# Performance work log

Hardware: AMD Instinct MI355X
Metric: run time of the kernel (lower is better)

The kernel has to match this reference:

```python
import jax, jax.numpy as jnp
import numpy as np

N_DEPTH = 16  # == serialization_depth init kwarg


def _normalize(v, axis):
    # F.normalize: v / max(||v||, 1e-12)
    return v / jnp.maximum(jnp.linalg.norm(v, axis=axis, keepdims=True), 1e-12)


def _weighted_mean(p, mask):
    # p: [B,N,1], mask: [B,N]
    n = jnp.sum(mask, axis=1, keepdims=True)[..., None]
    return jnp.sum(p * mask[..., None], axis=1, keepdims=True) / (n + 1e-9)


def _select_duplet(points, m, k1, k2):
    # pick 2 random valid points (argmin of rand + big penalty on masked-out) and average
    B, N, _ = points.shape
    def pick(k):
        s = jax.random.uniform(k, (B, N)) + (1.0 - m) * 1e9
        idx = jnp.argmin(s, axis=1)           # [B]
        return jnp.take_along_axis(points, idx[:, None, None], axis=1)  # [B,1,3]
    return (pick(k1) + pick(k2)) * 0.5


def _align(points, ml, mr, ks):
    pl = points - _select_duplet(points, ml, ks[0], ks[1])
    pr = points - _select_duplet(points, mr, ks[2], ks[3])
    return pl * ml[..., None] + pr * mr[..., None]


def _serialize(coords, mask, n_depth, key):
    B, N, _ = coords.shape
    inf = float(2 ** (n_depth // 2 + 3))
    s0 = 2 ** (n_depth // 2 + 1)
    # integer halving each step, exactly like score_scale // 2 in torch
    scales = jnp.asarray(np.array([s0 >> i for i in range(n_depth)], dtype=np.float32))
    keys = jax.random.split(key, n_depth * 5).reshape(n_depth, 5)

    total0 = jnp.zeros((B, N, 1), coords.dtype)
    oldABC0 = jnp.ones((B, 3, 1), coords.dtype)

    def step(carry, inp):
        points, oldABC, total = carry
        ks, scale = inp
        ABC = jax.random.normal(ks[0], (B, 3, 1), coords.dtype)
        angle = jnp.sum(_normalize(ABC, 1) * _normalize(oldABC, 1), axis=1, keepdims=True)
        sgn = jnp.sign(angle)
        sgn = jnp.where(sgn == 0, 1.0, sgn)
        ABC = ABC * sgn
        proj = points @ ABC                    # [B,N,1]
        proj = proj - _weighted_mean(proj, mask)
        score = jnp.sign(proj)                 # [B,N,1]
        total = total + score * scale
        ml = jnp.minimum(jax.nn.relu(-score[..., 0]), mask)
        mr = jnp.minimum(jax.nn.relu(score[..., 0]), mask)
        points = _align(points, ml, mr, ks[1:])
        return (points, ABC, total), None

    (_, _, total), _ = jax.lax.scan(step, (coords, oldABC0, total0), (keys, scales))
    total = total + inf * (1.0 - mask)[..., None]
    return jnp.argsort(total[..., 0], axis=1)  # [B,N]


def setup_inputs() -> dict:
    key = jax.random.key(0)
    k1, k2 = jax.random.split(key)
    B, N, D = 16, 8192, 256
    x = jax.random.normal(k1, (B, N, D), dtype=jnp.float32)
    x_coords = jax.random.normal(k2, (B, N, 3), dtype=jnp.float32)
    mask = jnp.ones((B, N), dtype=jnp.float32)
    return {"x": x, "x_coords": x_coords, "mask": mask}


def reference(x, x_coords, mask):
    key = jax.random.key(42)
    idx = _serialize(x_coords, mask, N_DEPTH, key)   # [B,N] int
    # reverse_indices: gather(arange, idx) == idx, then argsort
    rev = jnp.argsort(idx, axis=1)
    x_out = jnp.take_along_axis(x, idx[:, :, None], axis=1)
    return x_out, rev
```

## Files before the change

kernel.cpp:

```cpp
#include <hip/hip_runtime.h>
#include <stdint.h>

#pragma clang fp contract(off)

constexpr bool kPartitionable = true;

constexpr int B_ = 16;
constexpr int N_ = 8192;
constexpr int TPB = 1024;
constexpr int NSTEP = 10;

__device__ __forceinline__ void tf2x32(uint32_t k0, uint32_t k1,
                                       uint32_t x0, uint32_t x1,
                                       uint32_t& o0, uint32_t& o1) {
  uint32_t ks2 = k0 ^ k1 ^ 0x1BD11BDAu;
  x0 += k0; x1 += k1;
#define RND(r) { x0 += x1; x1 = (x1 << (r)) | (x1 >> (32 - (r))); x1 ^= x0; }
  RND(13) RND(15) RND(26) RND(6)   x0 += k1;  x1 += ks2 + 1u;
  RND(17) RND(29) RND(16) RND(24)  x0 += ks2; x1 += k0  + 2u;
  RND(13) RND(15) RND(26) RND(6)   x0 += k0;  x1 += k1  + 3u;
  RND(17) RND(29) RND(16) RND(24)  x0 += k1;  x1 += ks2 + 4u;
  RND(13) RND(15) RND(26) RND(6)   x0 += ks2; x1 += k0  + 5u;
#undef RND
  o0 = x0; o1 = x1;
}

__device__ __forceinline__ uint32_t rbits(uint32_t k0, uint32_t k1, uint32_t i) {
  uint32_t o0, o1;
  tf2x32(k0, k1, 0u, i, o0, o1);
  return o0 ^ o1;
}

__device__ __forceinline__ void derive_key(uint32_t j, uint32_t& k0, uint32_t& k1) {
  uint32_t o0, o1;
  tf2x32(0u, 42u, 0u, j, o0, o1);
  k0 = o0; k1 = o1;
}

__device__ __forceinline__ float u01_from_bits(uint32_t bits) {
  return __fsub_rn(__uint_as_float((bits >> 9) | 0x3f800000u), 1.0f);
}

__device__ __forceinline__ float xla_logf(float x) {
  uint32_t ix = __float_as_uint(x);
  int e = (int)((ix >> 23) & 0xffu) - 126;
  float m = __uint_as_float((ix & 0x007fffffu) | 0x3f000000u);
  float ef = (float)e;
  if (m < 0.707106781186547524f) {
    ef = __fsub_rn(ef, 1.0f);
    m = __fsub_rn(__fadd_rn(m, m), 1.0f);
  } else {
    m = __fsub_rn(m, 1.0f);
  }
  float z = __fmul_rn(m, m);
  float y = 7.0376836292e-2f;
  y = __fadd_rn(__fmul_rn(y, m), -1.1514610310e-1f);
  y = __fadd_rn(__fmul_rn(y, m),  1.1676998740e-1f);
  y = __fadd_rn(__fmul_rn(y, m), -1.2420140846e-1f);
  y = __fadd_rn(__fmul_rn(y, m),  1.4249322787e-1f);
  y = __fadd_rn(__fmul_rn(y, m), -1.6668057665e-1f);
  y = __fadd_rn(__fmul_rn(y, m),  2.0000714765e-1f);
  y = __fadd_rn(__fmul_rn(y, m), -2.4999993993e-1f);
  y = __fadd_rn(__fmul_rn(y, m),  3.3333331174e-1f);
  y = __fmul_rn(__fmul_rn(y, m), z);
  y = __fadd_rn(y, __fmul_rn(ef, -2.12194440e-4f));
  y = __fadd_rn(y, __fmul_rn(-0.5f, z));
  float r = __fadd_rn(m, y);
  r = __fadd_rn(r, __fmul_rn(ef, 0.693359375f));
  return r;
}

__device__ __forceinline__ float xla_log1p(float z) {
  if (fabsf(z) < 1e-4f)
    return __fmul_rn(__fadd_rn(__fmul_rn(-0.5f, z), 1.0f), z);
  return xla_logf(__fadd_rn(z, 1.0f));
}

__device__ __forceinline__ float erfinv_xla(float x) {
  float xx = __fmul_rn(x, x);
  float w = -xla_log1p(-xx);
  float p;
  if (w < 5.0f) {
    float ww = __fsub_rn(w, 2.5f);
    p = 2.81022636e-08f;
    p = __fadd_rn(__fmul_rn(p, ww),  3.43273939e-07f);
    p = __fadd_rn(__fmul_rn(p, ww), -3.5233877e-06f);
    p = __fadd_rn(__fmul_rn(p, ww), -4.39150654e-06f);
    p = __fadd_rn(__fmul_rn(p, ww),  0.00021858087f);
    p = __fadd_rn(__fmul_rn(p, ww), -0.00125372503f);
    p = __fadd_rn(__fmul_rn(p, ww), -0.00417768164f);
    p = __fadd_rn(__fmul_rn(p, ww),  0.246640727f);
    p = __fadd_rn(__fmul_rn(p, ww),  1.50140941f);
  } else {
    float ww = __fsub_rn(__fsqrt_rn(w), 3.0f);
    p = -0.000200214257f;
    p = __fadd_rn(__fmul_rn(p, ww),  0.000100950558f);
    p = __fadd_rn(__fmul_rn(p, ww),  0.00134934322f);
    p = __fadd_rn(__fmul_rn(p, ww), -0.00367342844f);
    p = __fadd_rn(__fmul_rn(p, ww),  0.00573950773f);
    p = __fadd_rn(__fmul_rn(p, ww), -0.0076224613f);
    p = __fadd_rn(__fmul_rn(p, ww),  0.00943887047f);
    p = __fadd_rn(__fmul_rn(p, ww),  1.00167406f);
    p = __fadd_rn(__fmul_rn(p, ww),  2.83297682f);
  }
  return __fmul_rn(p, x);
}

__global__ __launch_bounds__(TPB)
void rand_kernel(float* __restrict__ uni, float* __restrict__ abc) {
  const int blk = blockIdx.x;
  const int tid = threadIdx.x;
  if (blk < 640) {
    int b = blk / 40, r = blk % 40, t = r / 4, q = r % 4;
    uint32_t k0, k1;
    derive_key((uint32_t)(5 * t + 1 + q), k0, k1);
    float* dst = uni + (((size_t)b * NSTEP + t) * 4 + q) * (size_t)N_;
    float4 lo, hi;
    int n0 = 4 * tid, n1 = 4096 + 4 * tid;
    lo.x = u01_from_bits(rbits(k0, k1, (uint32_t)(b * N_ + n0 + 0)));
    lo.y = u01_from_bits(rbits(k0, k1, (uint32_t)(b * N_ + n0 + 1)));
    lo.z = u01_from_bits(rbits(k0, k1, (uint32_t)(b * N_ + n0 + 2)));
    lo.w = u01_from_bits(rbits(k0, k1, (uint32_t)(b * N_ + n0 + 3)));
    hi.x = u01_from_bits(rbits(k0, k1, (uint32_t)(b * N_ + n1 + 0)));
    hi.y = u01_from_bits(rbits(k0, k1, (uint32_t)(b * N_ + n1 + 1)));
    hi.z = u01_from_bits(rbits(k0, k1, (uint32_t)(b * N_ + n1 + 2)));
    hi.w = u01_from_bits(rbits(k0, k1, (uint32_t)(b * N_ + n1 + 3)));
    *(float4*)(dst + n0) = lo;
    *(float4*)(dst + n1) = hi;
  } else if (tid < 16) {
    const int b = tid;
    const float kLo = -0x1.fffffep-1f;
    const float kSqrt2 = 0x1.6a09e6p+0f;
    float o0 = 1.f, o1 = 1.f, o2 = 1.f;
    for (int t = 0; t < NSTEP; ++t) {
      uint32_t k0, k1;
      derive_key((uint32_t)(5 * t), k0, k1);
      float a[3];
#pragma unroll
      for (int c = 0; c < 3; ++c) {
        float f = u01_from_bits(rbits(k0, k1, (uint32_t)(b * 3 + c)));
        float u = __fadd_rn(__fmul_rn(f, 2.0f), kLo);
        u = fmaxf(kLo, u);
        a[c] = __fmul_rn(kSqrt2, erfinv_xla(u));
      }
      float na2 = __fadd_rn(__fadd_rn(__fmul_rn(a[0],a[0]),__fmul_rn(a[1],a[1])),__fmul_rn(a[2],a[2]));
      float no2 = __fadd_rn(__fadd_rn(__fmul_rn(o0,o0),__fmul_rn(o1,o1)),__fmul_rn(o2,o2));
      float nan_ = fmaxf(__fsqrt_rn(na2), 1e-12f);
      float non_ = fmaxf(__fsqrt_rn(no2), 1e-12f);
      float u0=__fdiv_rn(a[0],nan_), u1=__fdiv_rn(a[1],nan_), u2=__fdiv_rn(a[2],nan_);
      float v0=__fdiv_rn(o0,non_),  v1=__fdiv_rn(o1,non_),  v2=__fdiv_rn(o2,non_);
      float ang = __fadd_rn(__fadd_rn(__fmul_rn(u0,v0),__fmul_rn(u1,v1)),__fmul_rn(u2,v2));
      float sg = (ang > 0.f) ? 1.f : ((ang < 0.f) ? -1.f : 1.f);
      a[0]=__fmul_rn(a[0],sg); a[1]=__fmul_rn(a[1],sg); a[2]=__fmul_rn(a[2],sg);
      abc[b * 30 + t * 3 + 0] = a[0];
      abc[b * 30 + t * 3 + 1] = a[1];
      abc[b * 30 + t * 3 + 2] = a[2];
      o0 = a[0]; o1 = a[1]; o2 = a[2];
    }
  }
}

#define ACC4(v) { s = __fadd_rn(s, (v).x); s = __fadd_rn(s, (v).y); \
                  s = __fadd_rn(s, (v).z); s = __fadd_rn(s, (v).w); }

__device__ __forceinline__ float seq_sum_8192(const float4* v) {
  float4 a0=v[0],a1=v[1],a2=v[2],a3=v[3],a4=v[4],a5=v[5],a6=v[6],a7=v[7];
  float s = 0.f;
  for (int c = 0; c < 256; c += 2) {
    const int nb = (c + 1) << 3, na = (c + 2) << 3;
    float4 b0=v[nb+0],b1=v[nb+1],b2=v[nb+2],b3=v[nb+3];
    float4 b4=v[nb+4],b5=v[nb+5],b6=v[nb+6],b7=v[nb+7];
    ACC4(a0) ACC4(a1) ACC4(a2) ACC4(a3) ACC4(a4) ACC4(a5) ACC4(a6) ACC4(a7)
    a0=v[na+0];a1=v[na+1];a2=v[na+2];a3=v[na+3];
    a4=v[na+4];a5=v[na+5];a6=v[na+6];a7=v[na+7];
    ACC4(b0) ACC4(b1) ACC4(b2) ACC4(b3) ACC4(b4) ACC4(b5) ACC4(b6) ACC4(b7)
  }
  return s;
}

__global__ __launch_bounds__(TPB, 1)
void serialize_kernel(const float* __restrict__ coords, const float* __restrict__ mask,
                      const float* __restrict__ uni, const float* __restrict__ abc,
                      float* __restrict__ pts_ws, int* __restrict__ idx_ws,
                      float* __restrict__ rev_out) {
  const int b = blockIdx.x;
  const int tid = threadIdx.x;

  __shared__ __align__(16) float pm[N_ + 32];
  __shared__ float    pv[4][16];
  __shared__ int      pi[4][16];
  __shared__ float    s_abcs[NSTEP][3], s_dl[3], s_dr[3];
  __shared__ float    s_stash[48];
  __shared__ float    s_red[16];
  __shared__ float    s_mean, s_denom;

  float* pts = pts_ws + (size_t)b * N_ * 3;
  const float* cb = coords + (size_t)b * N_ * 3;
  const float* mb = mask + (size_t)b * N_;

  if (tid < 30) s_abcs[tid / 3][tid % 3] = abc[b * 30 + tid];

  float m_[8];
  {
    float4 m4a = *(const float4*)(mb + 4 * tid);
    float4 m4b = *(const float4*)(mb + 4096 + 4 * tid);
    m_[0]=m4a.x; m_[1]=m4a.y; m_[2]=m4a.z; m_[3]=m4a.w;
    m_[4]=m4b.x; m_[5]=m4b.y; m_[6]=m4b.z; m_[7]=m4b.w;
  }

  float p_[8][3];
  {
    const float4* cA = (const float4*)(cb + 12 * tid);
    const float4* cB = (const float4*)(cb + 12288 + 12 * tid);
    float4 v0=cA[0], v1=cA[1], v2=cA[2];
    p_[0][0]=v0.x; p_[0][1]=v0.y; p_[0][2]=v0.z;
    p_[1][0]=v0.w; p_[1][1]=v1.x; p_[1][2]=v1.y;
    p_[2][0]=v1.z; p_[2][1]=v1.w; p_[2][2]=v2.x;
    p_[3][0]=v2.y; p_[3][1]=v2.z; p_[3][2]=v2.w;
    float4 w0=cB[0], w1=cB[1], w2=cB[2];
    p_[4][0]=w0.x; p_[4][1]=w0.y; p_[4][2]=w0.z;
    p_[5][0]=w0.w; p_[5][1]=w1.x; p_[5][2]=w1.y;
    p_[6][0]=w1.z; p_[6][1]=w1.w; p_[6][2]=w2.x;
    p_[7][0]=w2.y; p_[7][1]=w2.z; p_[7][2]=w2.w;
    float4* dA = (float4*)(pts + 12 * tid);
    float4* dB = (float4*)(pts + 12288 + 12 * tid);
    dA[0]=v0; dA[1]=v1; dA[2]=v2;
    dB[0]=w0; dB[1]=w1; dB[2]=w2;
  }

  {
    float ds = 0.f;
#pragma unroll
    for (int e = 0; e < 8; ++e) ds = __fadd_rn(ds, m_[e]);
#pragma unroll
    for (int off = 32; off > 0; off >>= 1) ds = __fadd_rn(ds, __shfl_xor(ds, off));
    if ((tid & 63) == 0) s_red[tid >> 6] = ds;
  }
  __syncthreads();
  if (tid == 0) {
    float s = 0.f;
#pragma unroll
    for (int w = 0; w < 16; ++w) s = __fadd_rn(s, s_red[w]);
    s_denom = __fadd_rn(s, 1e-9f);
  }

  float tot_[8];
#pragma unroll
  for (int e = 0; e < 8; ++e) tot_[e] = 0.f;

  __syncthreads();

  float proj_[8], sc_[8];

  for (int t = 0; t < NSTEP; ++t) {
    const float A0 = s_abcs[t][0], A1 = s_abcs[t][1], A2 = s_abcs[t][2];

#pragma unroll
    for (int e = 0; e < 8; ++e)
      proj_[e] = __fadd_rn(__fadd_rn(__fmul_rn(p_[e][0], A0), __fmul_rn(p_[e][1], A1)),
                           __fmul_rn(p_[e][2], A2));
    {
      float4 w0, w1;
      w0.x=__fmul_rn(proj_[0],m_[0]); w0.y=__fmul_rn(proj_[1],m_[1]);
      w0.z=__fmul_rn(proj_[2],m_[2]); w0.w=__fmul_rn(proj_[3],m_[3]);
      w1.x=__fmul_rn(proj_[4],m_[4]); w1.y=__fmul_rn(proj_[5],m_[5]);
      w1.z=__fmul_rn(proj_[6],m_[6]); w1.w=__fmul_rn(proj_[7],m_[7]);
      ((float4*)pm)[tid] = w0;
      ((float4*)pm)[1024 + tid] = w1;
    }

    float4 fl[4], fh[4];
    {
      const float* ub = uni + (((size_t)b * NSTEP + t) * 4) * (size_t)N_;
#pragma unroll
      for (int q = 0; q < 4; ++q) {
        fl[q] = *(const float4*)(ub + (size_t)q * N_ + 4 * tid);
        fh[q] = *(const float4*)(ub + (size_t)q * N_ + 4096 + 4 * tid);
      }
    }
    __syncthreads();

    if (tid == 0) {
#pragma unroll
      for (int e = 0; e < 8; ++e) {
        s_stash[e*3+0]=p_[e][0]; s_stash[e*3+1]=p_[e][1]; s_stash[e*3+2]=p_[e][2];
        s_stash[24+e]=tot_[e];
        s_stash[32+e]=proj_[e];
        s_stash[40+e]=m_[e];
      }
      __builtin_amdgcn_s_setprio(1);
      float s = seq_sum_8192((const float4*)pm);
      __builtin_amdgcn_s_setprio(0);
      s_mean = __fdiv_rn(s, s_denom);
#pragma unroll
      for (int e = 0; e < 8; ++e) {
        p_[e][0]=s_stash[e*3+0]; p_[e][1]=s_stash[e*3+1]; p_[e][2]=s_stash[e*3+2];
        tot_[e]=s_stash[24+e];
        proj_[e]=s_stash[32+e];
        m_[e]=s_stash[40+e];
      }
    }
    __syncthreads();

    const float mean = s_mean;
    const float sca = (float)(512u >> t);
    float bv[4]; int bi_[4];
#pragma unroll
    for (int q = 0; q < 4; ++q) { bv[q] = 1e30f; bi_[q] = 0x7fffffff; }
#pragma unroll
    for (int e = 0; e < 8; ++e) {
      float d = __fsub_rn(proj_[e], mean);
      float s0 = (d > 0.f) ? 1.f : ((d < 0.f) ? -1.f : 0.f);
      sc_[e] = s0;
      tot_[e] = __fadd_rn(tot_[e], __fmul_rn(s0, sca));
      float mlv = fminf(fmaxf(-s0, 0.f), m_[e]);
      float mrv = fminf(fmaxf( s0, 0.f), m_[e]);
      int n = (e < 4) ? (4*tid + e) : (4096 + 4*tid + (e - 4));
#pragma unroll
      for (int q = 0; q < 4; ++q) {
        float meff = (q < 2) ? mlv : mrv;
        float fval;
        if (e < 4) fval = (e == 0 ? fl[q].x : e == 1 ? fl[q].y : e == 2 ? fl[q].z : fl[q].w);
        else       fval = (e == 4 ? fh[q].x : e == 5 ? fh[q].y : e == 6 ? fh[q].z : fh[q].w);
        float val = __fadd_rn(fval, __fmul_rn(__fsub_rn(1.0f, meff), 1e9f));
        if (val < bv[q] || (val == bv[q] && n < bi_[q])) { bv[q] = val; bi_[q] = n; }
      }
    }
#pragma unroll
    for (int off = 32; off > 0; off >>= 1) {
#pragma unroll
      for (int q = 0; q < 4; ++q) {
        float vv = __shfl_xor(bv[q], off);
        int   ii = __shfl_xor(bi_[q], off);
        if (vv < bv[q] || (vv == bv[q] && ii < bi_[q])) { bv[q] = vv; bi_[q] = ii; }
      }
    }
    if ((tid & 63) == 0) {
      int w = tid >> 6;
#pragma unroll
      for (int q = 0; q < 4; ++q) { pv[q][w] = bv[q]; pi[q][w] = bi_[q]; }
    }
    __syncthreads();

    if (tid < 64) {
      int w = tid & 15, q = tid >> 4;
      float v = pv[q][w]; int i = pi[q][w];
#pragma unroll
      for (int off = 1; off < 16; off <<= 1) {
        float vv = __shfl_xor(v, off);
        int   ii = __shfl_xor(i, off);
        if (vv < v || (vv == v && ii < i)) { v = vv; i = ii; }
      }
      int g0 = __shfl(i, 0), g1 = __shfl(i, 16), g2 = __shfl(i, 32), g3 = __shfl(i, 48);
      if (tid == 0) {
#pragma unroll
        for (int c = 0; c < 3; ++c) {
          s_dl[c] = __fmul_rn(__fadd_rn(pts[g0*3+c], pts[g1*3+c]), 0.5f);
          s_dr[c] = __fmul_rn(__fadd_rn(pts[g2*3+c], pts[g3*3+c]), 0.5f);
        }
      }
    }
    __syncthreads();

    {
      float dl0=s_dl[0], dl1=s_dl[1], dl2=s_dl[2];
      float dr0=s_dr[0], dr1=s_dr[1], dr2=s_dr[2];
#pragma unroll
      for (int e = 0; e < 8; ++e) {
        float s0 = sc_[e];
        float mlv = fminf(fmaxf(-s0, 0.f), m_[e]);
        float mrv = fminf(fmaxf( s0, 0.f), m_[e]);
        p_[e][0] = __fadd_rn(__fmul_rn(__fsub_rn(p_[e][0], dl0), mlv),
                             __fmul_rn(__fsub_rn(p_[e][0], dr0), mrv));
        p_[e][1] = __fadd_rn(__fmul_rn(__fsub_rn(p_[e][1], dl1), mlv),
                             __fmul_rn(__fsub_rn(p_[e][1], dr1), mrv));
        p_[e][2] = __fadd_rn(__fmul_rn(__fsub_rn(p_[e][2], dl2), mlv),
                             __fmul_rn(__fsub_rn(p_[e][2], dr2), mrv));
      }
      float4 v0, v1, v2;
      v0.x=p_[0][0]; v0.y=p_[0][1]; v0.z=p_[0][2]; v0.w=p_[1][0];
      v1.x=p_[1][1]; v1.y=p_[1][2]; v1.z=p_[2][0]; v1.w=p_[2][1];
      v2.x=p_[2][2]; v2.y=p_[3][0]; v2.z=p_[3][1]; v2.w=p_[3][2];
      float4* dA = (float4*)(pts + 12 * tid);
      dA[0]=v0; dA[1]=v1; dA[2]=v2;
      v0.x=p_[4][0]; v0.y=p_[4][1]; v0.z=p_[4][2]; v0.w=p_[5][0];
      v1.x=p_[5][1]; v1.y=p_[5][2]; v1.z=p_[6][0]; v1.w=p_[6][1];
      v2.x=p_[6][2]; v2.y=p_[7][0]; v2.z=p_[7][1]; v2.w=p_[7][2];
      float4* dB = (float4*)(pts + 12288 + 12 * tid);
      dB[0]=v0; dB[1]=v1; dB[2]=v2;
    }
  }

  uint32_t* keys = reinterpret_cast<uint32_t*>(pm);
  {
    uint32_t kk_[8];
#pragma unroll
    for (int e = 0; e < 8; ++e) {
      int n = (e < 4) ? (4*tid + e) : (4096 + 4*tid + (e - 4));
      float tf = __fadd_rn(tot_[e], __fmul_rn(2048.0f, __fsub_rn(1.0f, m_[e])));
      int bin = (int)tf + 1023;
      bin = min(max(bin, 0), 4095);
      kk_[e] = ((uint32_t)bin << 13) | (uint32_t)n;
    }
    uint4 u0, u1;
    u0.x=kk_[0]; u0.y=kk_[1]; u0.z=kk_[2]; u0.w=kk_[3];
    u1.x=kk_[4]; u1.y=kk_[5]; u1.z=kk_[6]; u1.w=kk_[7];
    ((uint4*)keys)[tid] = u0;
    ((uint4*)keys)[1024 + tid] = u1;
  }
  for (uint32_t kk = 2; kk <= (uint32_t)N_; kk <<= 1) {
    for (uint32_t j = kk >> 1; j > 0; j >>= 1) {
      __syncthreads();
#pragma unroll
      for (int r = 0; r < 4; ++r) {
        int pidx = tid + (r << 10);
        int i = ((pidx & ~((int)j - 1)) << 1) | (pidx & ((int)j - 1));
        int l = i | (int)j;
        uint32_t a = keys[i], c2 = keys[l];
        bool up = ((i & (int)kk) == 0);
        if ((a > c2) == up) { keys[i] = c2; keys[l] = a; }
      }
    }
  }
  __syncthreads();
#pragma unroll
  for (int r = 0; r < 8; ++r) {
    int pos = tid + (r << 10);
    uint32_t key = keys[pos];
    int n = (int)(key & 8191u);
    idx_ws[b * N_ + pos] = n;
    rev_out[b * N_ + n] = (float)pos;
  }
}

__global__ __launch_bounds__(256)
void gather_kernel(const float* __restrict__ x, const int* __restrict__ idx_ws,
                   float* __restrict__ out) {
  int row = blockIdx.x * 4 + (threadIdx.x >> 6);
  int lane = threadIdx.x & 63;
  int b = row >> 13;
  int n = idx_ws[row];
  const float4* src = reinterpret_cast<const float4*>(x + ((size_t)(b * N_ + n)) * 256);
  float4* dst = reinterpret_cast<float4*>(out + (size_t)row * 256);
  dst[lane] = src[lane];
}

extern "C" void kernel_launch(void* const* d_in, const int* in_sizes, int n_in,
                              void* d_out, int out_size, void* d_ws, size_t ws_size,
                              hipStream_t stream) {
  const float* x      = (const float*)d_in[0];
  const float* coords = (const float*)d_in[1];
  const float* mask   = (const float*)d_in[2];
  float* out = (float*)d_out;

  float* uni    = (float*)d_ws;
  float* abc    = uni + (size_t)B_ * NSTEP * 4 * N_;
  float* pts_ws = abc + 480;
  int*   idx_ws = (int*)(pts_ws + (size_t)B_ * N_ * 3);
  float* rev_out = out + (size_t)B_ * N_ * 256;

  rand_kernel<<<dim3(641), dim3(TPB), 0, stream>>>(uni, abc);
  serialize_kernel<<<dim3(B_), dim3(TPB), 0, stream>>>(coords, mask, uni, abc,
                                                       pts_ws, idx_ws, rev_out);
  gather_kernel<<<dim3(B_ * N_ / 4), dim3(256), 0, stream>>>(x, idx_ws, out);
}
```

Baseline: 546.8 us.

## Skip last-step duplet selection, stash uniforms in LDS, widen nontemporal gather

The last serialization step's align/duplet work does not affect the final order, so that step no longer generates or loads its random uniforms and exits the loop right after updating the totals. Thread 0 now also stashes its uniform registers in shared memory around the long sequential sum, to lower register pressure. The gather kernel uses 512-thread blocks and nontemporal loads and stores. The rand kernel launch and the workspace shrink to match, which cuts work in the RNG and serialize stages.

```diff
diff --git a/kernel.cpp b/kernel.cpp
--- a/kernel.cpp
+++ b/kernel.cpp
@@ -2,13 +2,13 @@
 #include <stdint.h>
 
 #pragma clang fp contract(off)
-
-constexpr bool kPartitionable = true;
 
 constexpr int B_ = 16;
 constexpr int N_ = 8192;
 constexpr int TPB = 1024;
 constexpr int NSTEP = 10;
+
+typedef float f32x4 __attribute__((ext_vector_type(4)));
 
 __device__ __forceinline__ void tf2x32(uint32_t k0, uint32_t k1,
                                        uint32_t x0, uint32_t x1,
@@ -110,11 +110,11 @@
 void rand_kernel(float* __restrict__ uni, float* __restrict__ abc) {
   const int blk = blockIdx.x;
   const int tid = threadIdx.x;
-  if (blk < 640) {
-    int b = blk / 40, r = blk % 40, t = r / 4, q = r % 4;
+  if (blk < 576) {
+    int b = blk / 36, r = blk % 36, t = r / 4, q = r % 4;
     uint32_t k0, k1;
     derive_key((uint32_t)(5 * t + 1 + q), k0, k1);
-    float* dst = uni + (((size_t)b * NSTEP + t) * 4 + q) * (size_t)N_;
+    float* dst = uni + (((size_t)b * (NSTEP - 1) + t) * 4 + q) * (size_t)N_;
     float4 lo, hi;
     int n0 = 4 * tid, n1 = 4096 + 4 * tid;
     lo.x = u01_from_bits(rbits(k0, k1, (uint32_t)(b * N_ + n0 + 0)));
@@ -190,7 +190,7 @@
   __shared__ float    pv[4][16];
   __shared__ int      pi[4][16];
   __shared__ float    s_abcs[NSTEP][3], s_dl[3], s_dr[3];
-  __shared__ float    s_stash[48];
+  __shared__ __align__(16) float s_stash[80];
   __shared__ float    s_red[16];
   __shared__ float    s_mean, s_denom;
 
@@ -253,6 +253,7 @@
   float proj_[8], sc_[8];
 
   for (int t = 0; t < NSTEP; ++t) {
+    const bool live = (t < NSTEP - 1);
     const float A0 = s_abcs[t][0], A1 = s_abcs[t][1], A2 = s_abcs[t][2];
 
 #pragma unroll
@@ -270,8 +271,8 @@
     }
 
     float4 fl[4], fh[4];
-    {
-      const float* ub = uni + (((size_t)b * NSTEP + t) * 4) * (size_t)N_;
+    if (live) {
+      const float* ub = uni + (((size_t)b * (NSTEP - 1) + t) * 4) * (size_t)N_;
 #pragma unroll
       for (int q = 0; q < 4; ++q) {
         fl[q] = *(const float4*)(ub + (size_t)q * N_ + 4 * tid);
@@ -288,6 +289,13 @@
         s_stash[32+e]=proj_[e];
         s_stash[40+e]=m_[e];
       }
+      if (live) {
+#pragma unroll
+        for (int q = 0; q < 4; ++q) {
+          *(float4*)&s_stash[48 + 8*q] = fl[q];
+          *(float4*)&s_stash[52 + 8*q] = fh[q];
+        }
+      }
       __builtin_amdgcn_s_setprio(1);
       float s = seq_sum_8192((const float4*)pm);
       __builtin_amdgcn_s_setprio(0);
@@ -299,6 +307,13 @@
         proj_[e]=s_stash[32+e];
         m_[e]=s_stash[40+e];
       }
+      if (live) {
+#pragma unroll
+        for (int q = 0; q < 4; ++q) {
+          fl[q] = *(const float4*)&s_stash[48 + 8*q];
+          fh[q] = *(const float4*)&s_stash[52 + 8*q];
+        }
+      }
     }
     __syncthreads();
 
@@ -313,19 +328,23 @@
       float s0 = (d > 0.f) ? 1.f : ((d < 0.f) ? -1.f : 0.f);
       sc_[e] = s0;
       tot_[e] = __fadd_rn(tot_[e], __fmul_rn(s0, sca));
-      float mlv = fminf(fmaxf(-s0, 0.f), m_[e]);
-      float mrv = fminf(fmaxf( s0, 0.f), m_[e]);
-      int n = (e < 4) ? (4*tid + e) : (4096 + 4*tid + (e - 4));
-#pragma unroll
-      for (int q = 0; q < 4; ++q) {
-        float meff = (q < 2) ? mlv : mrv;
-        float fval;
-        if (e < 4) fval = (e == 0 ? fl[q].x : e == 1 ? fl[q].y : e == 2 ? fl[q].z : fl[q].w);
-        else       fval = (e == 4 ? fh[q].x : e == 5 ? fh[q].y : e == 6 ? fh[q].z : fh[q].w);
-        float val = __fadd_rn(fval, __fmul_rn(__fsub_rn(1.0f, meff), 1e9f));
-        if (val < bv[q] || (val == bv[q] && n < bi_[q])) { bv[q] = val; bi_[q] = n; }
-      }
-    }
+      if (live) {
+        float mlv = fminf(fmaxf(-s0, 0.f), m_[e]);
+        float mrv = fminf(fmaxf( s0, 0.f), m_[e]);
+        int n = (e < 4) ? (4*tid + e) : (4096 + 4*tid + (e - 4));
+#pragma unroll
+        for (int q = 0; q < 4; ++q) {
+          float meff = (q < 2) ? mlv : mrv;
+          float fval;
+          if (e < 4) fval = (e == 0 ? fl[q].x : e == 1 ? fl[q].y : e == 2 ? fl[q].z : fl[q].w);
+          else       fval = (e == 4 ? fh[q].x : e == 5 ? fh[q].y : e == 6 ? fh[q].z : fh[q].w);
+          float val = __fadd_rn(fval, __fmul_rn(__fsub_rn(1.0f, meff), 1e9f));
+          if (val < bv[q] || (val == bv[q] && n < bi_[q])) { bv[q] = val; bi_[q] = n; }
+        }
+      }
+    }
+    if (!live) break;
+
 #pragma unroll
     for (int off = 32; off > 0; off >>= 1) {
 #pragma unroll
@@ -433,16 +452,17 @@
   }
 }
 
-__global__ __launch_bounds__(256)
+__global__ __launch_bounds__(512)
 void gather_kernel(const float* __restrict__ x, const int* __restrict__ idx_ws,
                    float* __restrict__ out) {
-  int row = blockIdx.x * 4 + (threadIdx.x >> 6);
+  int row = blockIdx.x * 8 + (threadIdx.x >> 6);
   int lane = threadIdx.x & 63;
   int b = row >> 13;
   int n = idx_ws[row];
-  const float4* src = reinterpret_cast<const float4*>(x + ((size_t)(b * N_ + n)) * 256);
-  float4* dst = reinterpret_cast<float4*>(out + (size_t)row * 256);
-  dst[lane] = src[lane];
+  const f32x4* src = reinterpret_cast<const f32x4*>(x + ((size_t)(b * N_ + n)) * 256);
+  f32x4* dst = reinterpret_cast<f32x4*>(out + (size_t)row * 256);
+  f32x4 v = __builtin_nontemporal_load(&src[lane]);
+  __builtin_nontemporal_store(v, &dst[lane]);
 }
 
 extern "C" void kernel_launch(void* const* d_in, const int* in_sizes, int n_in,
@@ -454,13 +474,13 @@
   float* out = (float*)d_out;
 
   float* uni    = (float*)d_ws;
-  float* abc    = uni + (size_t)B_ * NSTEP * 4 * N_;
+  float* abc    = uni + (size_t)B_ * (NSTEP - 1) * 4 * N_;
   float* pts_ws = abc + 480;
   int*   idx_ws = (int*)(pts_ws + (size_t)B_ * N_ * 3);
   float* rev_out = out + (size_t)B_ * N_ * 256;
 
-  rand_kernel<<<dim3(641), dim3(TPB), 0, stream>>>(uni, abc);
+  rand_kernel<<<dim3(577), dim3(TPB), 0, stream>>>(uni, abc);
   serialize_kernel<<<dim3(B_), dim3(TPB), 0, stream>>>(coords, mask, uni, abc,
                                                        pts_ws, idx_ws, rev_out);
-  gather_kernel<<<dim3(B_ * N_ / 4), dim3(256), 0, stream>>>(x, idx_ws, out);
-}
+  gather_kernel<<<dim3(B_ * N_ / 8), dim3(512), 0, stream>>>(x, idx_ws, out);
+}
```

After: 539.5 us. No clear change (-1.3%).
